# Performance work log

Hardware: AMD Instinct MI355X
Metric: run time of the kernel (lower is better)

## Reference

```python
import jax, jax.numpy as jnp
import numpy as np

EPS = 1e-6
DIAG_SIZE = 128  # triu band half-width (init kwarg diag_size)
NEG_INF = -1e9


def feature_map(x):
    # tanh feature map: phi(x) = tanh(x) + 1 (positive feature map)
    return jnp.tanh(x) + 1.0


def causal_dot_product(Q, K, V):
    # Q,K: [N,L,H,E], V: [N,L,H,D]
    # running KV state: S_l = sum_{s<=l} K_s V_s^T, materialized via cumsum
    kv = jnp.cumsum(jnp.einsum('nlhe,nlhd->nlhed', K, V), axis=1)  # [N,L,H,E,D]
    return jnp.einsum('nlhe,nlhed->nlhd', Q, kv)


def setup_inputs() -> dict:
    key = jax.random.key(0)
    k1, k2, k3 = jax.random.split(key, 3)
    N, L, H, E = 2, 2048, 8, 64
    queries = jax.random.normal(k1, (N, L, H, E), dtype=jnp.float32)
    keys = jax.random.normal(k2, (N, L, H, E), dtype=jnp.float32)
    values = jax.random.normal(k3, (N, L, H, E), dtype=jnp.float32)
    key_lengths_mask = jnp.ones((N, L), dtype=jnp.float32)  # all keys valid
    blend = jnp.full((1,), 0.9, dtype=jnp.float32)  # learned blend param (init 0.9)
    return {"queries": queries, "keys": keys, "values": values,
            "key_lengths_mask": key_lengths_mask, "blend": blend}


def reference(queries, keys, values, key_lengths_mask, blend):
    N, L, H, E = queries.shape
    # ---- linear attention path (kernel_1 = tanh, kernel_2 = 'none') ----
    Q1 = feature_map(queries)
    K1 = feature_map(keys) * key_lengths_mask[:, :, None, None]
    Z1 = 1.0 / (jnp.einsum('nlhi,nlhi->nlh', Q1, jnp.cumsum(K1, axis=1)) + EPS)
    LV = causal_dot_product(Q1, K1, values) * Z1[..., None]  # [N,L,H,D]
    # ---- full softmax attention path (banded by triu) ----
    softmax_temp = 1.0 / np.sqrt(E).astype(np.float32)
    QK = jnp.einsum('nlhe,nshe->nhls', queries, keys)  # [N,H,L,L]
    l_idx = jnp.arange(L)[:, None]
    s_idx = jnp.arange(L)[None, :]
    causal_add = jnp.where(s_idx <= l_idx, 0.0, NEG_INF)  # lower-triangular mask
    key_add = jnp.where(key_lengths_mask > 0, 0.0, NEG_INF)  # [N,L]
    logits = softmax_temp * (QK + causal_add[None, None] + key_add[:, None, None, :])
    A = jax.nn.softmax(logits, axis=-1)
    # torch.triu(A, diagonal=-diag_size): keep s >= l - diag_size
    band = s_idx >= (l_idx - DIAG_SIZE)
    A = jnp.where(band[None, None], A, 0.0)
    # dropout: eval mode (identity)
    SV = jnp.einsum('nhls,nshd->nlhd', A, values)
    b = blend[0]
    return b * SV + (1.0 - b) * LV
```

## Files before the change

### kernel.cpp

```cpp
#include <hip/hip_runtime.h>
#include <math.h>

#define N_ 2
#define L_ 2048
#define H_ 8
#define E_ 64
#define D_ 64
#define C_ 128
#define NC (L_/C_)
#define ROWSTRIDE (H_*E_)
#define TEMP 0.125f
#define EPS_F 1e-6f
#define NEG_INF_F (-1e9f)
#define CHUNK_WS (E_*D_ + E_)
#define NCHUNKS (N_*H_*NC)
#define TPAD 136
#define PPAD 72

typedef __attribute__((ext_vector_type(8))) short short8;
typedef __attribute__((ext_vector_type(4))) float f32x4;

__device__ __forceinline__ short f2bf(float x) {
  unsigned u = __float_as_uint(x);
  u += 0x7fffu + ((u >> 16) & 1u);
  return (short)(u >> 16);
}
__device__ __forceinline__ float bf2f(short s) {
  return __uint_as_float(((unsigned)(unsigned short)s) << 16);
}
__device__ __forceinline__ float tanh1f(float x) {
  float e = __expf(-2.f * x);
  return 2.f * __builtin_amdgcn_rcpf(1.f + e);
}

template <typename F>
__device__ __forceinline__ void stage_tile(short* __restrict__ dst,
                                           const float* __restrict__ src, F f) {
  const int t = threadIdx.x;
#pragma unroll
  for (int it = 0; it < 4; ++it) {
    int gi = it * 256 + t;
    int row = gi >> 3, g = gi & 7;
    const float* p = src + row * ROWSTRIDE + g * 8;
    float4 a = *(const float4*)p;
    float4 b = *(const float4*)(p + 4);
    float xs[8] = {a.x, a.y, a.z, a.w, b.x, b.y, b.z, b.w};
    short8 v;
#pragma unroll
    for (int j = 0; j < 8; ++j) v[j] = f2bf(f(xs[j], row));
    *(short8*)(dst + row * 64 + (g ^ (row & 7)) * 8) = v;
  }
}

__device__ __forceinline__ void stage_vT(short* __restrict__ vt,
                                         const float* __restrict__ Vbase) {
  const int t = threadIdx.x;
  const int d = t & 63, sb = t >> 6;
#pragma unroll
  for (int q = 0; q < 4; ++q) {
    int s0 = sb * 32 + q * 8;
    short8 v;
#pragma unroll
    for (int j = 0; j < 8; ++j) v[j] = f2bf(Vbase[(s0 + j) * ROWSTRIDE + d]);
    *(short8*)(vt + d * TPAD + (s0 >> 3) * 8) = v;
  }
}

__device__ __forceinline__ short8 frag_ld(const short* __restrict__ buf,
                                          int rowbase, int hf, int lane) {
  int r = rowbase + (lane & 15);
  int g = (hf * 4 + (lane >> 4)) ^ (r & 7);
  return *(const short8*)(buf + r * 64 + g * 8);
}
__device__ __forceinline__ short8 frag_ldT(const short* __restrict__ buf,
                                           int nbase, int g, int lane) {
  int r = nbase + (lane & 15);
  return *(const short8*)(buf + r * TPAD + g * 8);
}
__device__ __forceinline__ short8 frag_ldP(const short* __restrict__ buf,
                                           int rowbase, int ks, int lane) {
  int r = rowbase + (lane & 15);
  int g = ks * 4 + (lane >> 4);
  return *(const short8*)(buf + r * PPAD + g * 8);
}

__device__ __forceinline__ void pv_and_store(f32x4 acc[2][8], short* __restrict__ vt,
                                             short* __restrict__ pb,
                                             float* __restrict__ outp,
                                             int w, int lane, bool prevband) {
  const int col_lo = lane & 15;
  f32x4 accPV[2][4];
#pragma unroll
  for (int m = 0; m < 2; ++m)
#pragma unroll
    for (int nn = 0; nn < 4; ++nn) accPV[m][nn] = (f32x4){0.f, 0.f, 0.f, 0.f};
#pragma unroll
  for (int hh = 0; hh < 2; ++hh) {
#pragma unroll
    for (int m = 0; m < 2; ++m) {
      const int rbase = 32 * w + 16 * m + ((lane >> 4) << 2);
#pragma unroll
      for (int ch = 0; ch < 4; ++ch) {
        int ct = 4 * hh + ch, col = 16 * ct + col_lo;
#pragma unroll
        for (int reg = 0; reg < 4; ++reg) {
          float pp = acc[m][ct][reg];
          if (prevband && col < rbase + reg) pp = 0.f;
          pb[(rbase + reg) * PPAD + 16 * ch + col_lo] = f2bf(pp);
        }
      }
    }
#pragma unroll
    for (int ks = 0; ks < 2; ++ks) {
      short8 ap[2];
#pragma unroll
      for (int m = 0; m < 2; ++m) ap[m] = frag_ldP(pb, 32 * w + 16 * m, ks, lane);
      short8 bv[4];
#pragma unroll
      for (int nn = 0; nn < 4; ++nn)
        bv[nn] = frag_ldT(vt, 16 * nn, 8 * hh + ks * 4 + (lane >> 4), lane);
#pragma unroll
      for (int m = 0; m < 2; ++m)
#pragma unroll
        for (int nn = 0; nn < 4; ++nn)
          accPV[m][nn] = __builtin_amdgcn_mfma_f32_16x16x32_bf16(ap[m], bv[nn], accPV[m][nn], 0, 0, 0);
    }
  }
#pragma unroll
  for (int m = 0; m < 2; ++m) {
    const int rbase = 32 * w + 16 * m + ((lane >> 4) << 2);
#pragma unroll
    for (int nn = 0; nn < 4; ++nn)
#pragma unroll
      for (int reg = 0; reg < 4; ++reg)
        outp[(rbase + reg) * D_ + 16 * nn + col_lo] = accPV[m][nn][reg];
  }
}

extern "C" __global__ void __launch_bounds__(256, 3)
k_pre(const float* __restrict__ Q, const float* __restrict__ K,
      const float* __restrict__ V, const float* __restrict__ mask,
      float* __restrict__ ws, float* __restrict__ part,
      float* __restrict__ pvd, float* __restrict__ pvp,
      float* __restrict__ lvl, float* __restrict__ rsuml) {
  __shared__ short lds[17920];
  __shared__ float fmsk[C_];
  const int orig = blockIdx.x;
  const int swz = (orig & 7) * 336 + (orig >> 3);
  const int t = threadIdx.x;
  const int w = t >> 6, lane = t & 63;
  const int col_lo = lane & 15;

  if (swz < 2176) {
    const int nh = swz / 136;
    const int p = swz - nh * 136;
    int qb = (int)((sqrtf(8.f * p + 1.f) - 1.f) * 0.5f);
    while ((qb + 1) * (qb + 2) / 2 <= p) ++qb;
    while (qb * (qb + 1) / 2 > p) --qb;
    const int kb = p - qb * (qb + 1) / 2;
    const int h = nh & (H_ - 1), n = nh >> 3;
    const int koff = ((n * L_ + kb * C_) * H_ + h) * E_;

    stage_tile(lds, Q + ((n * L_ + qb * C_) * H_ + h) * E_,
               [](float x, int) { return x; });
    stage_tile(lds + 8192, K + koff, [](float x, int) { return x; });
    if (t < C_) fmsk[t] = mask[n * L_ + kb * C_ + t];
    __syncthreads();

    const int rowbase = w * 32;
    short8 afr[2][2];
#pragma unroll
    for (int m = 0; m < 2; ++m)
#pragma unroll
      for (int hh = 0; hh < 2; ++hh)
        afr[m][hh] = frag_ld(lds, rowbase + 16 * m, hh, lane);

    f32x4 acc[2][8];
#pragma unroll
    for (int m = 0; m < 2; ++m)
#pragma unroll
      for (int c = 0; c < 8; ++c) acc[m][c] = (f32x4){0.f, 0.f, 0.f, 0.f};
#pragma unroll
    for (int c = 0; c < 8; ++c) {
      short8 b0 = frag_ld(lds + 8192, 16 * c, 0, lane);
      short8 b1 = frag_ld(lds + 8192, 16 * c, 1, lane);
#pragma unroll
      for (int m = 0; m < 2; ++m) {
        acc[m][c] = __builtin_amdgcn_mfma_f32_16x16x32_bf16(afr[m][0], b0, acc[m][c], 0, 0, 0);
        acc[m][c] = __builtin_amdgcn_mfma_f32_16x16x32_bf16(afr[m][1], b1, acc[m][c], 0, 0, 0);
      }
    }

    const bool diag = (kb == qb), prev = (kb == qb - 1);
    float* pout = part + (size_t)(nh * NC + qb) * C_ * 16;
#pragma unroll
    for (int m = 0; m < 2; ++m) {
      const int rbase = rowbase + 16 * m + ((lane >> 4) << 2);
      float rs[4] = {0.f, 0.f, 0.f, 0.f};
#pragma unroll
      for (int c = 0; c < 8; ++c) {
        const int col = 16 * c + col_lo;
        const float madd = (fmsk[col] > 0.f) ? 0.f : NEG_INF_F;
#pragma unroll
        for (int reg = 0; reg < 4; ++reg) {
          float x = acc[m][c][reg] + madd;
          if (diag && col > rbase + reg) x += NEG_INF_F;
          float e = __expf(x * TEMP);
          acc[m][c][reg] = e;
          rs[reg] += e;
        }
      }
#pragma unroll
      for (int off = 1; off < 16; off <<= 1) {
#pragma unroll
        for (int reg = 0; reg < 4; ++reg) rs[reg] += __shfl_xor(rs[reg], off);
      }
      if (col_lo == 0) {
#pragma unroll
        for (int reg = 0; reg < 4; ++reg) pout[(rbase + reg) * 16 + kb] = rs[reg];
      }
    }

    if (diag || prev) {
      __syncthreads();
      stage_vT(lds, V + koff);
      __syncthreads();
      float* outp = (diag ? pvd : pvp) + (size_t)(nh * NC + qb) * (C_ * D_);
      pv_and_store(acc, lds, lds + 8704, outp, w, lane, prev);
    }
  } else if (swz < 2432) {
    const int id = swz - 2176;
    const int nh = id >> 4, c = id & 15;
    const int h = nh & (H_ - 1), n = nh >> 3;
    const int gbase = ((n * L_ + c * C_) * H_ + h) * E_;
    const int e = t & 63, sb = t >> 6;
    const int mbase = n * L_ + c * C_;
    short* k1T = lds;
    short* vT2 = lds + 8704;
#pragma unroll
    for (int q = 0; q < 4; ++q) {
      int s0 = sb * 32 + q * 8;
      short8 kk, vv;
#pragma unroll
      for (int j = 0; j < 8; ++j) {
        float kx = K[gbase + (s0 + j) * ROWSTRIDE + e];
        kk[j] = f2bf(tanh1f(kx) * mask[mbase + s0 + j]);
        vv[j] = f2bf(V[gbase + (s0 + j) * ROWSTRIDE + e]);
      }
      *(short8*)(k1T + e * TPAD + (s0 >> 3) * 8) = kk;
      *(short8*)(vT2 + e * TPAD + (s0 >> 3) * 8) = vv;
    }
    __syncthreads();

    f32x4 acc[4];
#pragma unroll
    for (int nn = 0; nn < 4; ++nn) acc[nn] = (f32x4){0.f, 0.f, 0.f, 0.f};
#pragma unroll
    for (int ks = 0; ks < 4; ++ks) {
      short8 a = frag_ldT(vT2, 16 * w, ks * 4 + (lane >> 4), lane);
#pragma unroll
      for (int nn = 0; nn < 4; ++nn) {
        short8 b = frag_ldT(k1T, 16 * nn, ks * 4 + (lane >> 4), lane);
        acc[nn] = __builtin_amdgcn_mfma_f32_16x16x32_bf16(a, b, acc[nn], 0, 0, 0);
      }
    }
    float* wsc = ws + (size_t)(nh * NC + c) * CHUNK_WS;
    const int drow = 16 * w + ((lane >> 4) << 2);
#pragma unroll
    for (int nn = 0; nn < 4; ++nn)
#pragma unroll
      for (int reg = 0; reg < 4; ++reg)
        wsc[(16 * nn + col_lo) * D_ + drow + reg] = acc[nn][reg];
    if (t < 64) {
      float s = 0.f;
#pragma unroll
      for (int g = 0; g < 16; ++g) {
        short8 v = *(const short8*)(k1T + t * TPAD + g * 8);
#pragma unroll
        for (int j = 0; j < 8; ++j) s += bf2f(v[j]);
      }
      wsc[E_ * D_ + t] = s;
    }
  } else {
    const int id = swz - 2432;
    const int nh = id >> 4, qb = id & 15;
    const int h = nh & (H_ - 1), n = nh >> 3;
    const int gbase = ((n * L_ + qb * C_) * H_ + h) * E_;
    const float* mrow = mask + n * L_ + qb * C_;

    stage_tile(lds, Q + gbase, [](float x, int) { return tanh1f(x); });
    stage_tile(lds + 8192, K + gbase,
               [mrow](float x, int row) { return tanh1f(x) * mrow[row]; });
    __syncthreads();

    const int rowbase = w * 32;
    short8 afr[2][2];
#pragma unroll
    for (int m = 0; m < 2; ++m)
#pragma unroll
      for (int hh = 0; hh < 2; ++hh)
        afr[m][hh] = frag_ld(lds, rowbase + 16 * m, hh, lane);

    f32x4 acc[2][8];
#pragma unroll
    for (int m = 0; m < 2; ++m)
#pragma unroll
      for (int c = 0; c < 8; ++c) acc[m][c] = (f32x4){0.f, 0.f, 0.f, 0.f};
#pragma unroll
    for (int c = 0; c < 8; ++c) {
      short8 b0 = frag_ld(lds + 8192, 16 * c, 0, lane);
      short8 b1 = frag_ld(lds + 8192, 16 * c, 1, lane);
#pragma unroll
      for (int m = 0; m < 2; ++m) {
        acc[m][c] = __builtin_amdgcn_mfma_f32_16x16x32_bf16(afr[m][0], b0, acc[m][c], 0, 0, 0);
        acc[m][c] = __builtin_amdgcn_mfma_f32_16x16x32_bf16(afr[m][1], b1, acc[m][c], 0, 0, 0);
      }
    }
    float* rout = rsuml + (size_t)(nh * NC + qb) * C_;
#pragma unroll
    for (int m = 0; m < 2; ++m) {
      const int rbase = rowbase + 16 * m + ((lane >> 4) << 2);
      float rs[4] = {0.f, 0.f, 0.f, 0.f};
#pragma unroll
      for (int c = 0; c < 8; ++c) {
        const int col = 16 * c + col_lo;
#pragma unroll
        for (int reg = 0; reg < 4; ++reg) {
          if (col <= rbase + reg) rs[reg] += acc[m][c][reg];
          else acc[m][c][reg] = 0.f;
        }
      }
#pragma unroll
      for (int off = 1; off < 16; off <<= 1) {
#pragma unroll
        for (int reg = 0; reg < 4; ++reg) rs[reg] += __shfl_xor(rs[reg], off);
      }
      if (col_lo == 0) {
#pragma unroll
        for (int reg = 0; reg < 4; ++reg) rout[rbase + reg] = rs[reg];
      }
    }
    __syncthreads();
    stage_vT(lds, V + gbase);
    __syncthreads();
    pv_and_store(acc, lds, lds + 8704,
                 lvl + (size_t)(nh * NC + qb) * (C_ * D_), w, lane, false);
  }
}

extern "C" __global__ void __launch_bounds__(256)
k_scan(float* __restrict__ ws) {
  const int bid = blockIdx.x;
  const int swz = (bid & 7) * 34 + (bid >> 3);
  const int nh = swz / 17, seg = swz - nh * 17;
  const int idx = seg * 256 + threadIdx.x;
  if (idx >= CHUNK_WS) return;
  float* base = ws + (size_t)nh * NC * CHUNK_WS + idx;
  float v[NC];
#pragma unroll
  for (int c = 0; c < NC; ++c) v[c] = base[(size_t)c * CHUNK_WS];
  float acc = 0.f;
#pragma unroll
  for (int c = 0; c < NC; ++c) {
    base[(size_t)c * CHUNK_WS] = acc;
    acc += v[c];
  }
}

extern "C" __global__ void __launch_bounds__(256)
k_fused(const float* __restrict__ Q, const float* __restrict__ blend,
        const float* __restrict__ ws, const float* __restrict__ part,
        const float* __restrict__ pvd, const float* __restrict__ pvp,
        const float* __restrict__ lvl, const float* __restrict__ rsuml,
        float* __restrict__ out) {
  __shared__ short kv[64 * TPAD];
  __shared__ float zlds[64];
  __shared__ float dinv[64];
  __shared__ float ksum[E_];

  const int orig = blockIdx.x;
  const int swz = (orig & 7) * 64 + (orig >> 3);
  const int rh = swz & 1, qb = (swz >> 1) & (NC - 1), nh = swz >> 5;
  const int h = nh & (H_ - 1), n = nh >> 3;
  const int t = threadIdx.x;
  const int w = t >> 6, lane = t & 63;
  const int rowbase = w * 16;
  const int col_lo = lane & 15;
  const int rb = rowbase + ((lane >> 4) << 2);
  const int rtile0 = rh * 64 + rb;
  const int qgbase = ((n * L_ + qb * C_ + rh * 64) * H_ + h) * E_;
  const float* wsc = ws + (size_t)(nh * NC + qb) * CHUNK_WS;
  const float bl = blend[0];
  const float ob = 1.f - bl;
  const int d = t & 63;
  const size_t tb = (size_t)(nh * NC + qb) * (C_ * D_);

  short8 af1[2];
  {
    const float* qp = Q + qgbase + (rowbase + (lane & 15)) * ROWSTRIDE;
#pragma unroll
    for (int kh = 0; kh < 2; ++kh) {
      int c0 = (kh * 4 + (lane >> 4)) * 8;
      float4 a = *(const float4*)(qp + c0);
      float4 b = *(const float4*)(qp + c0 + 4);
      float xs[8] = {a.x, a.y, a.z, a.w, b.x, b.y, b.z, b.w};
#pragma unroll
      for (int j = 0; j < 8; ++j) af1[kh][j] = f2bf(tanh1f(xs[j]));
    }
  }
  {
    int eb = t >> 6;
#pragma unroll
    for (int q = 0; q < 2; ++q) {
      int e0 = eb * 16 + q * 8;
      short8 v;
#pragma unroll
      for (int j = 0; j < 8; ++j) v[j] = f2bf(wsc[(e0 + j) * D_ + d]);
      *(short8*)(kv + d * TPAD + (e0 >> 3) * 8) = v;
    }
  }
  if (t < 64) {
    ksum[t] = wsc[E_ * D_ + t];
    const float* pb = part + ((size_t)(nh * NC + qb) * C_ + rh * 64 + t) * 16;
    float4 a = *(const float4*)pb, b = *(const float4*)(pb + 4);
    float4 c = *(const float4*)(pb + 8), d4 = *(const float4*)(pb + 12);
    float vv[16] = {a.x, a.y, a.z, a.w, b.x, b.y, b.z, b.w,
                    c.x, c.y, c.z, c.w, d4.x, d4.y, d4.z, d4.w};
    float s = 0.f;
#pragma unroll
    for (int j = 0; j < 16; ++j) s += (j <= qb) ? vv[j] : 0.f;
    dinv[t] = 1.f / s;
  }
  float rsv[4];
#pragma unroll
  for (int reg = 0; reg < 4; ++reg)
    rsv[reg] = rsuml[(size_t)(nh * NC + qb) * C_ + rtile0 + reg];
  float lvv[4][4], pvv[4][4];
#pragma unroll
  for (int nn = 0; nn < 4; ++nn)
#pragma unroll
    for (int reg = 0; reg < 4; ++reg) {
      size_t a = tb + (size_t)(rtile0 + reg) * D_ + 16 * nn + col_lo;
      lvv[nn][reg] = lvl[a];
      float pd = pvd[a];
      pvv[nn][reg] = (qb > 0) ? pd + pvp[a] : pd;
    }
  __syncthreads();

  {
    float zz = 0.f;
#pragma unroll
    for (int kh = 0; kh < 2; ++kh) {
      int cb = (kh * 4 + (lane >> 4)) * 8;
#pragma unroll
      for (int j = 0; j < 8; ++j) zz += bf2f(af1[kh][j]) * ksum[cb + j];
    }
    zz += __shfl_xor(zz, 16);
    zz += __shfl_xor(zz, 32);
    if (lane < 16) zlds[rowbase + lane] = zz;
  }
  f32x4 accL[4];
#pragma unroll
  for (int nn = 0; nn < 4; ++nn) accL[nn] = (f32x4){0.f, 0.f, 0.f, 0.f};
#pragma unroll
  for (int ks = 0; ks < 2; ++ks) {
    short8 bf[4];
#pragma unroll
    for (int nn = 0; nn < 4; ++nn)
      bf[nn] = frag_ldT(kv, 16 * nn, ks * 4 + (lane >> 4), lane);
#pragma unroll
    for (int nn = 0; nn < 4; ++nn)
      accL[nn] = __builtin_amdgcn_mfma_f32_16x16x32_bf16(af1[ks], bf[nn], accL[nn], 0, 0, 0);
  }

  float zrf[4], sdv[4];
#pragma unroll
  for (int reg = 0; reg < 4; ++reg) {
    zrf[reg] = ob / (zlds[rb + reg] + rsv[reg] + EPS_F);
    sdv[reg] = bl * dinv[rb + reg];
  }
#pragma unroll
  for (int nn = 0; nn < 4; ++nn)
#pragma unroll
    for (int reg = 0; reg < 4; ++reg)
      out[qgbase + (rb + reg) * ROWSTRIDE + 16 * nn + col_lo] =
          zrf[reg] * (accL[nn][reg] + lvv[nn][reg]) + sdv[reg] * pvv[nn][reg];
}

extern "C" void kernel_launch(void* const* d_in, const int* in_sizes, int n_in,
                              void* d_out, int out_size, void* d_ws, size_t ws_size,
                              hipStream_t stream) {
  (void)in_sizes; (void)n_in; (void)out_size; (void)ws_size;
  const float* Q = (const float*)d_in[0];
  const float* K = (const float*)d_in[1];
  const float* V = (const float*)d_in[2];
  const float* mask = (const float*)d_in[3];
  const float* blend = (const float*)d_in[4];
  float* out = (float*)d_out;
  float* ws = (float*)d_ws;
  float* part  = ws + (size_t)NCHUNKS * CHUNK_WS;
  float* pvd   = part + (size_t)NCHUNKS * C_ * 16;
  float* pvp   = pvd + (size_t)NCHUNKS * C_ * D_;
  float* lvl   = pvp + (size_t)NCHUNKS * C_ * D_;
  float* rsuml = lvl + (size_t)NCHUNKS * C_ * D_;

  k_pre<<<dim3(2688), dim3(256), 0, stream>>>(Q, K, V, mask, ws, part, pvd, pvp, lvl, rsuml);
  k_scan<<<dim3(272), dim3(256), 0, stream>>>(ws);
  k_fused<<<dim3(N_ * H_ * NC * 2), dim3(256), 0, stream>>>(Q, blend, ws, part, pvd, pvp, lvl, rsuml, out);
}
```

Baseline: 55.90 us.

## Interleave score MFMA, exp and PV per column half to cut registers

Restructures k_pre so the QK^T product is computed one 16-column tile at a time, immediately exponentiated and written to LDS as bf16, then multiplied by V for each 64-column half. This replaces the full 2x8 accumulator array and the separate pv_and_store pass. V is staged up front into a dedicated LDS buffer alongside Q and K, which removes the extra barriers and the serialized V staging. The block-to-work mapping is also regrouped per head (168 blocks each) rather than by task type, and the launch_bounds occupancy hint is dropped. Peak register pressure should fall, but LDS use per block rises, which may limit occupancy.

```diff
diff --git a/kernel.cpp b/kernel.cpp
--- a/kernel.cpp
+++ b/kernel.cpp
@@ -84,159 +84,128 @@
   return *(const short8*)(buf + r * PPAD + g * 8);
 }
 
-__device__ __forceinline__ void pv_and_store(f32x4 acc[2][8], short* __restrict__ vt,
-                                             short* __restrict__ pb,
-                                             float* __restrict__ outp,
-                                             int w, int lane, bool prevband) {
-  const int col_lo = lane & 15;
-  f32x4 accPV[2][4];
-#pragma unroll
-  for (int m = 0; m < 2; ++m)
-#pragma unroll
-    for (int nn = 0; nn < 4; ++nn) accPV[m][nn] = (f32x4){0.f, 0.f, 0.f, 0.f};
-#pragma unroll
-  for (int hh = 0; hh < 2; ++hh) {
-#pragma unroll
-    for (int m = 0; m < 2; ++m) {
-      const int rbase = 32 * w + 16 * m + ((lane >> 4) << 2);
-#pragma unroll
-      for (int ch = 0; ch < 4; ++ch) {
-        int ct = 4 * hh + ch, col = 16 * ct + col_lo;
-#pragma unroll
-        for (int reg = 0; reg < 4; ++reg) {
-          float pp = acc[m][ct][reg];
-          if (prevband && col < rbase + reg) pp = 0.f;
-          pb[(rbase + reg) * PPAD + 16 * ch + col_lo] = f2bf(pp);
-        }
-      }
-    }
-#pragma unroll
-    for (int ks = 0; ks < 2; ++ks) {
-      short8 ap[2];
-#pragma unroll
-      for (int m = 0; m < 2; ++m) ap[m] = frag_ldP(pb, 32 * w + 16 * m, ks, lane);
-      short8 bv[4];
-#pragma unroll
-      for (int nn = 0; nn < 4; ++nn)
-        bv[nn] = frag_ldT(vt, 16 * nn, 8 * hh + ks * 4 + (lane >> 4), lane);
-#pragma unroll
-      for (int m = 0; m < 2; ++m)
-#pragma unroll
-        for (int nn = 0; nn < 4; ++nn)
-          accPV[m][nn] = __builtin_amdgcn_mfma_f32_16x16x32_bf16(ap[m], bv[nn], accPV[m][nn], 0, 0, 0);
-    }
-  }
-#pragma unroll
-  for (int m = 0; m < 2; ++m) {
-    const int rbase = 32 * w + 16 * m + ((lane >> 4) << 2);
-#pragma unroll
-    for (int nn = 0; nn < 4; ++nn)
-#pragma unroll
-      for (int reg = 0; reg < 4; ++reg)
-        outp[(rbase + reg) * D_ + 16 * nn + col_lo] = accPV[m][nn][reg];
-  }
-}
-
-extern "C" __global__ void __launch_bounds__(256, 3)
+extern "C" __global__ void __launch_bounds__(256)
 k_pre(const float* __restrict__ Q, const float* __restrict__ K,
       const float* __restrict__ V, const float* __restrict__ mask,
       float* __restrict__ ws, float* __restrict__ part,
       float* __restrict__ pvd, float* __restrict__ pvp,
       float* __restrict__ lvl, float* __restrict__ rsuml) {
-  __shared__ short lds[17920];
+  __shared__ short ldsA[9216];
+  __shared__ short ldsB[8192];
+  __shared__ short ldsC[8704];
   __shared__ float fmsk[C_];
   const int orig = blockIdx.x;
   const int swz = (orig & 7) * 336 + (orig >> 3);
+  const int nh = swz / 168;
+  const int r = swz - nh * 168;
+  const int h = nh & (H_ - 1), n = nh >> 3;
   const int t = threadIdx.x;
   const int w = t >> 6, lane = t & 63;
   const int col_lo = lane & 15;
 
-  if (swz < 2176) {
-    const int nh = swz / 136;
-    const int p = swz - nh * 136;
+  if (r < 136) {
+    const int p = r;
     int qb = (int)((sqrtf(8.f * p + 1.f) - 1.f) * 0.5f);
     while ((qb + 1) * (qb + 2) / 2 <= p) ++qb;
     while (qb * (qb + 1) / 2 > p) --qb;
     const int kb = p - qb * (qb + 1) / 2;
-    const int h = nh & (H_ - 1), n = nh >> 3;
+    const bool diag = (kb == qb), prev = (kb == qb - 1), band = diag || prev;
     const int koff = ((n * L_ + kb * C_) * H_ + h) * E_;
 
-    stage_tile(lds, Q + ((n * L_ + qb * C_) * H_ + h) * E_,
+    stage_tile(ldsA, Q + ((n * L_ + qb * C_) * H_ + h) * E_,
                [](float x, int) { return x; });
-    stage_tile(lds + 8192, K + koff, [](float x, int) { return x; });
+    stage_tile(ldsB, K + koff, [](float x, int) { return x; });
+    if (band) stage_vT(ldsC, V + koff);
     if (t < C_) fmsk[t] = mask[n * L_ + kb * C_ + t];
     __syncthreads();
 
-    const int rowbase = w * 32;
     short8 afr[2][2];
 #pragma unroll
     for (int m = 0; m < 2; ++m)
 #pragma unroll
-      for (int hh = 0; hh < 2; ++hh)
-        afr[m][hh] = frag_ld(lds, rowbase + 16 * m, hh, lane);
-
-    f32x4 acc[2][8];
+      for (int hf = 0; hf < 2; ++hf)
+        afr[m][hf] = frag_ld(ldsA, w * 32 + 16 * m, hf, lane);
+    __syncthreads();
+
+    float rs[2][4] = {};
+    f32x4 accPV[2][4];
 #pragma unroll
     for (int m = 0; m < 2; ++m)
 #pragma unroll
-      for (int c = 0; c < 8; ++c) acc[m][c] = (f32x4){0.f, 0.f, 0.f, 0.f};
-#pragma unroll
-    for (int c = 0; c < 8; ++c) {
-      short8 b0 = frag_ld(lds + 8192, 16 * c, 0, lane);
-      short8 b1 = frag_ld(lds + 8192, 16 * c, 1, lane);
+      for (int nn = 0; nn < 4; ++nn) accPV[m][nn] = (f32x4){0.f, 0.f, 0.f, 0.f};
+
+#pragma unroll
+    for (int hh = 0; hh < 2; ++hh) {
+#pragma unroll
+      for (int cc = 0; cc < 4; ++cc) {
+        const int ct = hh * 4 + cc;
+        short8 b0 = frag_ld(ldsB, 16 * ct, 0, lane);
+        short8 b1 = frag_ld(ldsB, 16 * ct, 1, lane);
+        const int col = 16 * ct + col_lo;
+        const float madd = (fmsk[col] > 0.f) ? 0.f : NEG_INF_F;
+#pragma unroll
+        for (int m = 0; m < 2; ++m) {
+          f32x4 c = (f32x4){0.f, 0.f, 0.f, 0.f};
+          c = __builtin_amdgcn_mfma_f32_16x16x32_bf16(afr[m][0], b0, c, 0, 0, 0);
+          c = __builtin_amdgcn_mfma_f32_16x16x32_bf16(afr[m][1], b1, c, 0, 0, 0);
+          const int rbase = w * 32 + 16 * m + ((lane >> 4) << 2);
+#pragma unroll
+          for (int reg = 0; reg < 4; ++reg) {
+            float x = c[reg] + madd;
+            if (diag && col > rbase + reg) x += NEG_INF_F;
+            float e = __expf(x * TEMP);
+            rs[m][reg] += e;
+            if (band) {
+              if (prev && col < rbase + reg) e = 0.f;
+              ldsA[(rbase + reg) * PPAD + cc * 16 + col_lo] = f2bf(e);
+            }
+          }
+        }
+      }
+      if (band) {
+#pragma unroll
+        for (int ks = 0; ks < 2; ++ks) {
+          short8 ap0 = frag_ldP(ldsA, w * 32, ks, lane);
+          short8 ap1 = frag_ldP(ldsA, w * 32 + 16, ks, lane);
+#pragma unroll
+          for (int nn = 0; nn < 4; ++nn) {
+            short8 bv = frag_ldT(ldsC, 16 * nn, 8 * hh + ks * 4 + (lane >> 4), lane);
+            accPV[0][nn] = __builtin_amdgcn_mfma_f32_16x16x32_bf16(ap0, bv, accPV[0][nn], 0, 0, 0);
+            accPV[1][nn] = __builtin_amdgcn_mfma_f32_16x16x32_bf16(ap1, bv, accPV[1][nn], 0, 0, 0);
+          }
+        }
+      }
+    }
+    float* pout = part + (size_t)(nh * NC + qb) * C_ * 16;
+#pragma unroll
+    for (int m = 0; m < 2; ++m) {
+#pragma unroll
+      for (int off = 1; off < 16; off <<= 1)
+#pragma unroll
+        for (int reg = 0; reg < 4; ++reg) rs[m][reg] += __shfl_xor(rs[m][reg], off);
+      if (col_lo == 0) {
+        const int rbase = w * 32 + 16 * m + ((lane >> 4) << 2);
+#pragma unroll
+        for (int reg = 0; reg < 4; ++reg) pout[(rbase + reg) * 16 + kb] = rs[m][reg];
+      }
+    }
+    if (band) {
+      float* outp = (diag ? pvd : pvp) + (size_t)(nh * NC + qb) * (C_ * D_);
 #pragma unroll
       for (int m = 0; m < 2; ++m) {
-        acc[m][c] = __builtin_amdgcn_mfma_f32_16x16x32_bf16(afr[m][0], b0, acc[m][c], 0, 0, 0);
-        acc[m][c] = __builtin_amdgcn_mfma_f32_16x16x32_bf16(afr[m][1], b1, acc[m][c], 0, 0, 0);
-      }
-    }
-
-    const bool diag = (kb == qb), prev = (kb == qb - 1);
-    float* pout = part + (size_t)(nh * NC + qb) * C_ * 16;
-#pragma unroll
-    for (int m = 0; m < 2; ++m) {
-      const int rbase = rowbase + 16 * m + ((lane >> 4) << 2);
-      float rs[4] = {0.f, 0.f, 0.f, 0.f};
-#pragma unroll
-      for (int c = 0; c < 8; ++c) {
-        const int col = 16 * c + col_lo;
-        const float madd = (fmsk[col] > 0.f) ? 0.f : NEG_INF_F;
-#pragma unroll
-        for (int reg = 0; reg < 4; ++reg) {
-          float x = acc[m][c][reg] + madd;
-          if (diag && col > rbase + reg) x += NEG_INF_F;
-          float e = __expf(x * TEMP);
-          acc[m][c][reg] = e;
-          rs[reg] += e;
-        }
-      }
-#pragma unroll
-      for (int off = 1; off < 16; off <<= 1) {
-#pragma unroll
-        for (int reg = 0; reg < 4; ++reg) rs[reg] += __shfl_xor(rs[reg], off);
-      }
-      if (col_lo == 0) {
-#pragma unroll
-        for (int reg = 0; reg < 4; ++reg) pout[(rbase + reg) * 16 + kb] = rs[reg];
-      }
-    }
-
-    if (diag || prev) {
-      __syncthreads();
-      stage_vT(lds, V + koff);
-      __syncthreads();
-      float* outp = (diag ? pvd : pvp) + (size_t)(nh * NC + qb) * (C_ * D_);
-      pv_and_store(acc, lds, lds + 8704, outp, w, lane, prev);
-    }
-  } else if (swz < 2432) {
-    const int id = swz - 2176;
-    const int nh = id >> 4, c = id & 15;
-    const int h = nh & (H_ - 1), n = nh >> 3;
+        const int rbase = w * 32 + 16 * m + ((lane >> 4) << 2);
+#pragma unroll
+        for (int nn = 0; nn < 4; ++nn)
+#pragma unroll
+          for (int reg = 0; reg < 4; ++reg)
+            outp[(rbase + reg) * D_ + 16 * nn + col_lo] = accPV[m][nn][reg];
+      }
+    }
+  } else if (r < 152) {
+    const int c = r - 136;
     const int gbase = ((n * L_ + c * C_) * H_ + h) * E_;
     const int e = t & 63, sb = t >> 6;
     const int mbase = n * L_ + c * C_;
-    short* k1T = lds;
-    short* vT2 = lds + 8704;
 #pragma unroll
     for (int q = 0; q < 4; ++q) {
       int s0 = sb * 32 + q * 8;
@@ -247,8 +216,8 @@
         kk[j] = f2bf(tanh1f(kx) * mask[mbase + s0 + j]);
         vv[j] = f2bf(V[gbase + (s0 + j) * ROWSTRIDE + e]);
       }
-      *(short8*)(k1T + e * TPAD + (s0 >> 3) * 8) = kk;
-      *(short8*)(vT2 + e * TPAD + (s0 >> 3) * 8) = vv;
+      *(short8*)(ldsA + e * TPAD + (s0 >> 3) * 8) = kk;
+      *(short8*)(ldsC + e * TPAD + (s0 >> 3) * 8) = vv;
     }
     __syncthreads();
 
@@ -257,10 +226,10 @@
     for (int nn = 0; nn < 4; ++nn) acc[nn] = (f32x4){0.f, 0.f, 0.f, 0.f};
 #pragma unroll
     for (int ks = 0; ks < 4; ++ks) {
-      short8 a = frag_ldT(vT2, 16 * w, ks * 4 + (lane >> 4), lane);
+      short8 a = frag_ldT(ldsC, 16 * w, ks * 4 + (lane >> 4), lane);
 #pragma unroll
       for (int nn = 0; nn < 4; ++nn) {
-        short8 b = frag_ldT(k1T, 16 * nn, ks * 4 + (lane >> 4), lane);
+        short8 b = frag_ldT(ldsA, 16 * nn, ks * 4 + (lane >> 4), lane);
         acc[nn] = __builtin_amdgcn_mfma_f32_16x16x32_bf16(a, b, acc[nn], 0, 0, 0);
       }
     }
@@ -275,76 +244,96 @@
       float s = 0.f;
 #pragma unroll
       for (int g = 0; g < 16; ++g) {
-        short8 v = *(const short8*)(k1T + t * TPAD + g * 8);
+        short8 v = *(const short8*)(ldsA + t * TPAD + g * 8);
 #pragma unroll
         for (int j = 0; j < 8; ++j) s += bf2f(v[j]);
       }
       wsc[E_ * D_ + t] = s;
     }
   } else {
-    const int id = swz - 2432;
-    const int nh = id >> 4, qb = id & 15;
-    const int h = nh & (H_ - 1), n = nh >> 3;
+    const int qb = r - 152;
     const int gbase = ((n * L_ + qb * C_) * H_ + h) * E_;
     const float* mrow = mask + n * L_ + qb * C_;
 
-    stage_tile(lds, Q + gbase, [](float x, int) { return tanh1f(x); });
-    stage_tile(lds + 8192, K + gbase,
+    stage_tile(ldsA, Q + gbase, [](float x, int) { return tanh1f(x); });
+    stage_tile(ldsB, K + gbase,
                [mrow](float x, int row) { return tanh1f(x) * mrow[row]; });
+    stage_vT(ldsC, V + gbase);
     __syncthreads();
 
-    const int rowbase = w * 32;
     short8 afr[2][2];
 #pragma unroll
     for (int m = 0; m < 2; ++m)
 #pragma unroll
-      for (int hh = 0; hh < 2; ++hh)
-        afr[m][hh] = frag_ld(lds, rowbase + 16 * m, hh, lane);
-
-    f32x4 acc[2][8];
+      for (int hf = 0; hf < 2; ++hf)
+        afr[m][hf] = frag_ld(ldsA, w * 32 + 16 * m, hf, lane);
+    __syncthreads();
+
+    float rs[2][4] = {};
+    f32x4 accPV[2][4];
 #pragma unroll
     for (int m = 0; m < 2; ++m)
 #pragma unroll
-      for (int c = 0; c < 8; ++c) acc[m][c] = (f32x4){0.f, 0.f, 0.f, 0.f};
-#pragma unroll
-    for (int c = 0; c < 8; ++c) {
-      short8 b0 = frag_ld(lds + 8192, 16 * c, 0, lane);
-      short8 b1 = frag_ld(lds + 8192, 16 * c, 1, lane);
-#pragma unroll
-      for (int m = 0; m < 2; ++m) {
-        acc[m][c] = __builtin_amdgcn_mfma_f32_16x16x32_bf16(afr[m][0], b0, acc[m][c], 0, 0, 0);
-        acc[m][c] = __builtin_amdgcn_mfma_f32_16x16x32_bf16(afr[m][1], b1, acc[m][c], 0, 0, 0);
+      for (int nn = 0; nn < 4; ++nn) accPV[m][nn] = (f32x4){0.f, 0.f, 0.f, 0.f};
+
+#pragma unroll
+    for (int hh = 0; hh < 2; ++hh) {
+#pragma unroll
+      for (int cc = 0; cc < 4; ++cc) {
+        const int ct = hh * 4 + cc;
+        short8 b0 = frag_ld(ldsB, 16 * ct, 0, lane);
+        short8 b1 = frag_ld(ldsB, 16 * ct, 1, lane);
+        const int col = 16 * ct + col_lo;
+#pragma unroll
+        for (int m = 0; m < 2; ++m) {
+          f32x4 c = (f32x4){0.f, 0.f, 0.f, 0.f};
+          c = __builtin_amdgcn_mfma_f32_16x16x32_bf16(afr[m][0], b0, c, 0, 0, 0);
+          c = __builtin_amdgcn_mfma_f32_16x16x32_bf16(afr[m][1], b1, c, 0, 0, 0);
+          const int rbase = w * 32 + 16 * m + ((lane >> 4) << 2);
+#pragma unroll
+          for (int reg = 0; reg < 4; ++reg) {
+            float v = c[reg];
+            if (col <= rbase + reg) rs[m][reg] += v;
+            else v = 0.f;
+            ldsA[(rbase + reg) * PPAD + cc * 16 + col_lo] = f2bf(v);
+          }
+        }
+      }
+#pragma unroll
+      for (int ks = 0; ks < 2; ++ks) {
+        short8 ap0 = frag_ldP(ldsA, w * 32, ks, lane);
+        short8 ap1 = frag_ldP(ldsA, w * 32 + 16, ks, lane);
+#pragma unroll
+        for (int nn = 0; nn < 4; ++nn) {
+          short8 bv = frag_ldT(ldsC, 16 * nn, 8 * hh + ks * 4 + (lane >> 4), lane);
+          accPV[0][nn] = __builtin_amdgcn_mfma_f32_16x16x32_bf16(ap0, bv, accPV[0][nn], 0, 0, 0);
+          accPV[1][nn] = __builtin_amdgcn_mfma_f32_16x16x32_bf16(ap1, bv, accPV[1][nn], 0, 0, 0);
+        }
       }
     }
     float* rout = rsuml + (size_t)(nh * NC + qb) * C_;
 #pragma unroll
     for (int m = 0; m < 2; ++m) {
-      const int rbase = rowbase + 16 * m + ((lane >> 4) << 2);
-      float rs[4] = {0.f, 0.f, 0.f, 0.f};
-#pragma unroll
-      for (int c = 0; c < 8; ++c) {
-        const int col = 16 * c + col_lo;
-#pragma unroll
-        for (int reg = 0; reg < 4; ++reg) {
-          if (col <= rbase + reg) rs[reg] += acc[m][c][reg];
-          else acc[m][c][reg] = 0.f;
-        }
-      }
-#pragma unroll
-      for (int off = 1; off < 16; off <<= 1) {
-#pragma unroll
-        for (int reg = 0; reg < 4; ++reg) rs[reg] += __shfl_xor(rs[reg], off);
-      }
+#pragma unroll
+      for (int off = 1; off < 16; off <<= 1)
+#pragma unroll
+        for (int reg = 0; reg < 4; ++reg) rs[m][reg] += __shfl_xor(rs[m][reg], off);
       if (col_lo == 0) {
-#pragma unroll
-        for (int reg = 0; reg < 4; ++reg) rout[rbase + reg] = rs[reg];
-      }
-    }
-    __syncthreads();
-    stage_vT(lds, V + gbase);
-    __syncthreads();
-    pv_and_store(acc, lds, lds + 8704,
-                 lvl + (size_t)(nh * NC + qb) * (C_ * D_), w, lane, false);
+        const int rbase = w * 32 + 16 * m + ((lane >> 4) << 2);
+#pragma unroll
+        for (int reg = 0; reg < 4; ++reg) rout[rbase + reg] = rs[m][reg];
+      }
+    }
+    float* outp = lvl + (size_t)(nh * NC + qb) * (C_ * D_);
+#pragma unroll
+    for (int m = 0; m < 2; ++m) {
+      const int rbase = w * 32 + 16 * m + ((lane >> 4) << 2);
+#pragma unroll
+      for (int nn = 0; nn < 4; ++nn)
+#pragma unroll
+        for (int reg = 0; reg < 4; ++reg)
+          outp[(rbase + reg) * D_ + 16 * nn + col_lo] = accPV[m][nn][reg];
+    }
   }
 }
 
@@ -368,11 +357,11 @@
 }
 
 extern "C" __global__ void __launch_bounds__(256)
-k_fused(const float* __restrict__ Q, const float* __restrict__ blend,
-        const float* __restrict__ ws, const float* __restrict__ part,
-        const float* __restrict__ pvd, const float* __restrict__ pvp,
-        const float* __restrict__ lvl, const float* __restrict__ rsuml,
-        float* __restrict__ out) {
+k_comb(const float* __restrict__ Q, const float* __restrict__ blend,
+       const float* __restrict__ ws, const float* __restrict__ part,
+       const float* __restrict__ pvd, const float* __restrict__ pvp,
+       const float* __restrict__ lvl, const float* __restrict__ rsuml,
+       float* __restrict__ out) {
   __shared__ short kv[64 * TPAD];
   __shared__ float zlds[64];
   __shared__ float dinv[64];
@@ -506,5 +495,5 @@
 
   k_pre<<<dim3(2688), dim3(256), 0, stream>>>(Q, K, V, mask, ws, part, pvd, pvp, lvl, rsuml);
   k_scan<<<dim3(272), dim3(256), 0, stream>>>(ws);
-  k_fused<<<dim3(N_ * H_ * NC * 2), dim3(256), 0, stream>>>(Q, blend, ws, part, pvd, pvp, lvl, rsuml, out);
-}
+  k_comb<<<dim3(512), dim3(256), 0, stream>>>(Q, blend, ws, part, pvd, pvp, lvl, rsuml, out);
+}
```

Result: no change. 55.06 us (-1.5%).

## Split band and intra-chunk linear PV work into separate half-tile kernel

Applied to the files above, without the earlier changes.

Moves the banded softmax PV (diagonal and previous chunk) and the intra-chunk linear-attention PV out of k_pre into a new k_bandlin kernel. That kernel processes 64-row half tiles, loading Q fragments straight from global memory. k_pre now only computes softmax row-sum partials and chunk KV states, with lighter blocks and no occupancy hint. The aim is to even out load imbalance, since a few heavy blocks in the triangular grid did extra PV work. The cost is an extra kernel launch, and K and V tiles are re-staged in both kernels.

```diff
diff --git a/kernel.cpp b/kernel.cpp
--- a/kernel.cpp
+++ b/kernel.cpp
@@ -84,69 +84,15 @@
   return *(const short8*)(buf + r * PPAD + g * 8);
 }
 
-__device__ __forceinline__ void pv_and_store(f32x4 acc[2][8], short* __restrict__ vt,
-                                             short* __restrict__ pb,
-                                             float* __restrict__ outp,
-                                             int w, int lane, bool prevband) {
-  const int col_lo = lane & 15;
-  f32x4 accPV[2][4];
-#pragma unroll
-  for (int m = 0; m < 2; ++m)
-#pragma unroll
-    for (int nn = 0; nn < 4; ++nn) accPV[m][nn] = (f32x4){0.f, 0.f, 0.f, 0.f};
-#pragma unroll
-  for (int hh = 0; hh < 2; ++hh) {
-#pragma unroll
-    for (int m = 0; m < 2; ++m) {
-      const int rbase = 32 * w + 16 * m + ((lane >> 4) << 2);
-#pragma unroll
-      for (int ch = 0; ch < 4; ++ch) {
-        int ct = 4 * hh + ch, col = 16 * ct + col_lo;
-#pragma unroll
-        for (int reg = 0; reg < 4; ++reg) {
-          float pp = acc[m][ct][reg];
-          if (prevband && col < rbase + reg) pp = 0.f;
-          pb[(rbase + reg) * PPAD + 16 * ch + col_lo] = f2bf(pp);
-        }
-      }
-    }
-#pragma unroll
-    for (int ks = 0; ks < 2; ++ks) {
-      short8 ap[2];
-#pragma unroll
-      for (int m = 0; m < 2; ++m) ap[m] = frag_ldP(pb, 32 * w + 16 * m, ks, lane);
-      short8 bv[4];
-#pragma unroll
-      for (int nn = 0; nn < 4; ++nn)
-        bv[nn] = frag_ldT(vt, 16 * nn, 8 * hh + ks * 4 + (lane >> 4), lane);
-#pragma unroll
-      for (int m = 0; m < 2; ++m)
-#pragma unroll
-        for (int nn = 0; nn < 4; ++nn)
-          accPV[m][nn] = __builtin_amdgcn_mfma_f32_16x16x32_bf16(ap[m], bv[nn], accPV[m][nn], 0, 0, 0);
-    }
-  }
-#pragma unroll
-  for (int m = 0; m < 2; ++m) {
-    const int rbase = 32 * w + 16 * m + ((lane >> 4) << 2);
-#pragma unroll
-    for (int nn = 0; nn < 4; ++nn)
-#pragma unroll
-      for (int reg = 0; reg < 4; ++reg)
-        outp[(rbase + reg) * D_ + 16 * nn + col_lo] = accPV[m][nn][reg];
-  }
-}
-
-extern "C" __global__ void __launch_bounds__(256, 3)
+extern "C" __global__ void __launch_bounds__(256)
 k_pre(const float* __restrict__ Q, const float* __restrict__ K,
       const float* __restrict__ V, const float* __restrict__ mask,
-      float* __restrict__ ws, float* __restrict__ part,
-      float* __restrict__ pvd, float* __restrict__ pvp,
-      float* __restrict__ lvl, float* __restrict__ rsuml) {
-  __shared__ short lds[17920];
+      float* __restrict__ ws, float* __restrict__ part) {
+  __shared__ short ldsA[64 * TPAD];
+  __shared__ short ldsB[64 * TPAD];
   __shared__ float fmsk[C_];
   const int orig = blockIdx.x;
-  const int swz = (orig & 7) * 336 + (orig >> 3);
+  const int swz = (orig & 7) * 304 + (orig >> 3);
   const int t = threadIdx.x;
   const int w = t >> 6, lane = t & 63;
   const int col_lo = lane & 15;
@@ -159,11 +105,11 @@
     while (qb * (qb + 1) / 2 > p) --qb;
     const int kb = p - qb * (qb + 1) / 2;
     const int h = nh & (H_ - 1), n = nh >> 3;
-    const int koff = ((n * L_ + kb * C_) * H_ + h) * E_;
-
-    stage_tile(lds, Q + ((n * L_ + qb * C_) * H_ + h) * E_,
+
+    stage_tile(ldsA, Q + ((n * L_ + qb * C_) * H_ + h) * E_,
                [](float x, int) { return x; });
-    stage_tile(lds + 8192, K + koff, [](float x, int) { return x; });
+    stage_tile(ldsB, K + ((n * L_ + kb * C_) * H_ + h) * E_,
+               [](float x, int) { return x; });
     if (t < C_) fmsk[t] = mask[n * L_ + kb * C_ + t];
     __syncthreads();
 
@@ -173,17 +119,18 @@
     for (int m = 0; m < 2; ++m)
 #pragma unroll
       for (int hh = 0; hh < 2; ++hh)
-        afr[m][hh] = frag_ld(lds, rowbase + 16 * m, hh, lane);
+        afr[m][hh] = frag_ld(ldsA, rowbase + 16 * m, hh, lane);
 
     f32x4 acc[2][8];
 #pragma unroll
     for (int m = 0; m < 2; ++m)
 #pragma unroll
       for (int c = 0; c < 8; ++c) acc[m][c] = (f32x4){0.f, 0.f, 0.f, 0.f};
+
 #pragma unroll
     for (int c = 0; c < 8; ++c) {
-      short8 b0 = frag_ld(lds + 8192, 16 * c, 0, lane);
-      short8 b1 = frag_ld(lds + 8192, 16 * c, 1, lane);
+      short8 b0 = frag_ld(ldsB, 16 * c, 0, lane);
+      short8 b1 = frag_ld(ldsB, 16 * c, 1, lane);
 #pragma unroll
       for (int m = 0; m < 2; ++m) {
         acc[m][c] = __builtin_amdgcn_mfma_f32_16x16x32_bf16(afr[m][0], b0, acc[m][c], 0, 0, 0);
@@ -191,7 +138,7 @@
       }
     }
 
-    const bool diag = (kb == qb), prev = (kb == qb - 1);
+    const bool diag = (kb == qb);
     float* pout = part + (size_t)(nh * NC + qb) * C_ * 16;
 #pragma unroll
     for (int m = 0; m < 2; ++m) {
@@ -205,9 +152,7 @@
         for (int reg = 0; reg < 4; ++reg) {
           float x = acc[m][c][reg] + madd;
           if (diag && col > rbase + reg) x += NEG_INF_F;
-          float e = __expf(x * TEMP);
-          acc[m][c][reg] = e;
-          rs[reg] += e;
+          rs[reg] += __expf(x * TEMP);
         }
       }
 #pragma unroll
@@ -220,23 +165,13 @@
         for (int reg = 0; reg < 4; ++reg) pout[(rbase + reg) * 16 + kb] = rs[reg];
       }
     }
-
-    if (diag || prev) {
-      __syncthreads();
-      stage_vT(lds, V + koff);
-      __syncthreads();
-      float* outp = (diag ? pvd : pvp) + (size_t)(nh * NC + qb) * (C_ * D_);
-      pv_and_store(acc, lds, lds + 8704, outp, w, lane, prev);
-    }
-  } else if (swz < 2432) {
+  } else {
     const int id = swz - 2176;
     const int nh = id >> 4, c = id & 15;
     const int h = nh & (H_ - 1), n = nh >> 3;
     const int gbase = ((n * L_ + c * C_) * H_ + h) * E_;
     const int e = t & 63, sb = t >> 6;
     const int mbase = n * L_ + c * C_;
-    short* k1T = lds;
-    short* vT2 = lds + 8704;
 #pragma unroll
     for (int q = 0; q < 4; ++q) {
       int s0 = sb * 32 + q * 8;
@@ -247,8 +182,8 @@
         kk[j] = f2bf(tanh1f(kx) * mask[mbase + s0 + j]);
         vv[j] = f2bf(V[gbase + (s0 + j) * ROWSTRIDE + e]);
       }
-      *(short8*)(k1T + e * TPAD + (s0 >> 3) * 8) = kk;
-      *(short8*)(vT2 + e * TPAD + (s0 >> 3) * 8) = vv;
+      *(short8*)(ldsA + e * TPAD + (s0 >> 3) * 8) = kk;
+      *(short8*)(ldsB + e * TPAD + (s0 >> 3) * 8) = vv;
     }
     __syncthreads();
 
@@ -257,10 +192,10 @@
     for (int nn = 0; nn < 4; ++nn) acc[nn] = (f32x4){0.f, 0.f, 0.f, 0.f};
 #pragma unroll
     for (int ks = 0; ks < 4; ++ks) {
-      short8 a = frag_ldT(vT2, 16 * w, ks * 4 + (lane >> 4), lane);
+      short8 a = frag_ldT(ldsB, 16 * w, ks * 4 + (lane >> 4), lane);
 #pragma unroll
       for (int nn = 0; nn < 4; ++nn) {
-        short8 b = frag_ldT(k1T, 16 * nn, ks * 4 + (lane >> 4), lane);
+        short8 b = frag_ldT(ldsA, 16 * nn, ks * 4 + (lane >> 4), lane);
         acc[nn] = __builtin_amdgcn_mfma_f32_16x16x32_bf16(a, b, acc[nn], 0, 0, 0);
       }
     }
@@ -275,77 +210,153 @@
       float s = 0.f;
 #pragma unroll
       for (int g = 0; g < 16; ++g) {
-        short8 v = *(const short8*)(k1T + t * TPAD + g * 8);
+        short8 v = *(const short8*)(ldsA + t * TPAD + g * 8);
 #pragma unroll
         for (int j = 0; j < 8; ++j) s += bf2f(v[j]);
       }
       wsc[E_ * D_ + t] = s;
     }
+  }
+}
+
+extern "C" __global__ void __launch_bounds__(256)
+k_bandlin(const float* __restrict__ Q, const float* __restrict__ K,
+          const float* __restrict__ V, const float* __restrict__ mask,
+          float* __restrict__ pvd, float* __restrict__ pvp,
+          float* __restrict__ lvl, float* __restrict__ rsuml) {
+  __shared__ short kbuf[C_ * 64];
+  __shared__ short vt[64 * TPAD];
+  __shared__ short pbuf[64 * PPAD];
+  __shared__ float fmsk[C_];
+  const int orig = blockIdx.x;
+  const int swz = (orig & 7) * 192 + (orig >> 3);
+  const int nh = swz / 96, r = swz - nh * 96;
+  const int h = nh & (H_ - 1), n = nh >> 3;
+  const int t = threadIdx.x;
+  const int w = t >> 6, lane = t & 63;
+  const int col_lo = lane & 15;
+  const int prow = w * 16 + ((lane >> 4) << 2);
+
+  const bool isband = (r < 64);
+  int qb, rh, kb;
+  bool diag = false;
+  if (isband) {
+    qb = r >> 2; rh = (r >> 1) & 1;
+    const int slot = r & 1;
+    diag = (slot == 0);
+    kb = diag ? qb : qb - 1;
+    if (!diag && qb == 0) return;
   } else {
-    const int id = swz - 2432;
-    const int nh = id >> 4, qb = id & 15;
-    const int h = nh & (H_ - 1), n = nh >> 3;
-    const int gbase = ((n * L_ + qb * C_) * H_ + h) * E_;
-    const float* mrow = mask + n * L_ + qb * C_;
-
-    stage_tile(lds, Q + gbase, [](float x, int) { return tanh1f(x); });
-    stage_tile(lds + 8192, K + gbase,
+    const int r2 = r - 64;
+    qb = r2 >> 1; rh = r2 & 1; kb = qb;
+  }
+
+  const int koff = ((n * L_ + kb * C_) * H_ + h) * E_;
+  const int qoff = ((n * L_ + qb * C_ + rh * 64) * H_ + h) * E_;
+  const float* mrow = mask + n * L_ + kb * C_;
+
+  if (isband) {
+    stage_tile(kbuf, K + koff, [](float x, int) { return x; });
+    if (t < C_) fmsk[t] = mrow[t];
+  } else {
+    stage_tile(kbuf, K + koff,
                [mrow](float x, int row) { return tanh1f(x) * mrow[row]; });
-    __syncthreads();
-
-    const int rowbase = w * 32;
-    short8 afr[2][2];
-#pragma unroll
-    for (int m = 0; m < 2; ++m)
-#pragma unroll
-      for (int hh = 0; hh < 2; ++hh)
-        afr[m][hh] = frag_ld(lds, rowbase + 16 * m, hh, lane);
-
-    f32x4 acc[2][8];
-#pragma unroll
-    for (int m = 0; m < 2; ++m)
-#pragma unroll
-      for (int c = 0; c < 8; ++c) acc[m][c] = (f32x4){0.f, 0.f, 0.f, 0.f};
-#pragma unroll
-    for (int c = 0; c < 8; ++c) {
-      short8 b0 = frag_ld(lds + 8192, 16 * c, 0, lane);
-      short8 b1 = frag_ld(lds + 8192, 16 * c, 1, lane);
-#pragma unroll
-      for (int m = 0; m < 2; ++m) {
-        acc[m][c] = __builtin_amdgcn_mfma_f32_16x16x32_bf16(afr[m][0], b0, acc[m][c], 0, 0, 0);
-        acc[m][c] = __builtin_amdgcn_mfma_f32_16x16x32_bf16(afr[m][1], b1, acc[m][c], 0, 0, 0);
-      }
-    }
-    float* rout = rsuml + (size_t)(nh * NC + qb) * C_;
-#pragma unroll
-    for (int m = 0; m < 2; ++m) {
-      const int rbase = rowbase + 16 * m + ((lane >> 4) << 2);
-      float rs[4] = {0.f, 0.f, 0.f, 0.f};
-#pragma unroll
-      for (int c = 0; c < 8; ++c) {
-        const int col = 16 * c + col_lo;
-#pragma unroll
-        for (int reg = 0; reg < 4; ++reg) {
-          if (col <= rbase + reg) rs[reg] += acc[m][c][reg];
-          else acc[m][c][reg] = 0.f;
-        }
-      }
-#pragma unroll
-      for (int off = 1; off < 16; off <<= 1) {
-#pragma unroll
-        for (int reg = 0; reg < 4; ++reg) rs[reg] += __shfl_xor(rs[reg], off);
-      }
-      if (col_lo == 0) {
-#pragma unroll
-        for (int reg = 0; reg < 4; ++reg) rout[rbase + reg] = rs[reg];
-      }
-    }
-    __syncthreads();
-    stage_vT(lds, V + gbase);
-    __syncthreads();
-    pv_and_store(acc, lds, lds + 8704,
-                 lvl + (size_t)(nh * NC + qb) * (C_ * D_), w, lane, false);
-  }
+  }
+  stage_vT(vt, V + koff);
+  __syncthreads();
+
+  short8 af[2];
+  {
+    const float* qp = Q + qoff + (w * 16 + (lane & 15)) * ROWSTRIDE;
+#pragma unroll
+    for (int kh = 0; kh < 2; ++kh) {
+      int c0 = (kh * 4 + (lane >> 4)) * 8;
+      float4 a = *(const float4*)(qp + c0);
+      float4 b = *(const float4*)(qp + c0 + 4);
+      float xs[8] = {a.x, a.y, a.z, a.w, b.x, b.y, b.z, b.w};
+#pragma unroll
+      for (int j = 0; j < 8; ++j)
+        af[kh][j] = isband ? f2bf(xs[j]) : f2bf(tanh1f(xs[j]));
+    }
+  }
+
+  f32x4 acc[8];
+#pragma unroll
+  for (int ct = 0; ct < 8; ++ct) acc[ct] = (f32x4){0.f, 0.f, 0.f, 0.f};
+#pragma unroll
+  for (int ct = 0; ct < 8; ++ct) {
+    short8 b0 = frag_ld(kbuf, 16 * ct, 0, lane);
+    short8 b1 = frag_ld(kbuf, 16 * ct, 1, lane);
+    acc[ct] = __builtin_amdgcn_mfma_f32_16x16x32_bf16(af[0], b0, acc[ct], 0, 0, 0);
+    acc[ct] = __builtin_amdgcn_mfma_f32_16x16x32_bf16(af[1], b1, acc[ct], 0, 0, 0);
+  }
+
+  const int rowc = rh * 64 + prow;
+  float rs[4] = {0.f, 0.f, 0.f, 0.f};
+#pragma unroll
+  for (int ct = 0; ct < 8; ++ct) {
+    const int col = 16 * ct + col_lo;
+    if (isband) {
+      const float madd = (fmsk[col] > 0.f) ? 0.f : NEG_INF_F;
+#pragma unroll
+      for (int reg = 0; reg < 4; ++reg) {
+        float x = acc[ct][reg] + madd;
+        if (diag && col > rowc + reg) x += NEG_INF_F;
+        float e = __expf(x * TEMP);
+        if (!diag && col < rowc + reg) e = 0.f;
+        acc[ct][reg] = e;
+      }
+    } else {
+#pragma unroll
+      for (int reg = 0; reg < 4; ++reg) {
+        float v = acc[ct][reg];
+        if (col <= rowc + reg) rs[reg] += v;
+        else v = 0.f;
+        acc[ct][reg] = v;
+      }
+    }
+  }
+  if (!isband) {
+#pragma unroll
+    for (int off = 1; off < 16; off <<= 1)
+#pragma unroll
+      for (int reg = 0; reg < 4; ++reg) rs[reg] += __shfl_xor(rs[reg], off);
+    if (col_lo == 0) {
+      float* rout = rsuml + (size_t)(nh * NC + qb) * C_;
+#pragma unroll
+      for (int reg = 0; reg < 4; ++reg) rout[rowc + reg] = rs[reg];
+    }
+  }
+
+  f32x4 acc2[4];
+#pragma unroll
+  for (int nn = 0; nn < 4; ++nn) acc2[nn] = (f32x4){0.f, 0.f, 0.f, 0.f};
+#pragma unroll
+  for (int hh = 0; hh < 2; ++hh) {
+#pragma unroll
+    for (int cc = 0; cc < 4; ++cc) {
+      const int ct = 4 * hh + cc, colh = 16 * cc + col_lo;
+#pragma unroll
+      for (int reg = 0; reg < 4; ++reg)
+        pbuf[(prow + reg) * PPAD + colh] = f2bf(acc[ct][reg]);
+    }
+#pragma unroll
+    for (int ks = 0; ks < 2; ++ks) {
+      short8 ap = frag_ldP(pbuf, w * 16, ks, lane);
+#pragma unroll
+      for (int nn = 0; nn < 4; ++nn) {
+        short8 bv = frag_ldT(vt, 16 * nn, 8 * hh + ks * 4 + (lane >> 4), lane);
+        acc2[nn] = __builtin_amdgcn_mfma_f32_16x16x32_bf16(ap, bv, acc2[nn], 0, 0, 0);
+      }
+    }
+  }
+
+  float* outp = (isband ? (diag ? pvd : pvp) : lvl) + (size_t)(nh * NC + qb) * (C_ * D_);
+#pragma unroll
+  for (int nn = 0; nn < 4; ++nn)
+#pragma unroll
+    for (int reg = 0; reg < 4; ++reg)
+      outp[(size_t)(rowc + reg) * D_ + 16 * nn + col_lo] = acc2[nn][reg];
 }
 
 extern "C" __global__ void __launch_bounds__(256)
@@ -368,11 +379,11 @@
 }
 
 extern "C" __global__ void __launch_bounds__(256)
-k_fused(const float* __restrict__ Q, const float* __restrict__ blend,
-        const float* __restrict__ ws, const float* __restrict__ part,
-        const float* __restrict__ pvd, const float* __restrict__ pvp,
-        const float* __restrict__ lvl, const float* __restrict__ rsuml,
-        float* __restrict__ out) {
+k_comb(const float* __restrict__ Q, const float* __restrict__ blend,
+       const float* __restrict__ ws, const float* __restrict__ part,
+       const float* __restrict__ pvd, const float* __restrict__ pvp,
+       const float* __restrict__ lvl, const float* __restrict__ rsuml,
+       float* __restrict__ out) {
   __shared__ short kv[64 * TPAD];
   __shared__ float zlds[64];
   __shared__ float dinv[64];
@@ -504,7 +515,8 @@
   float* lvl   = pvp + (size_t)NCHUNKS * C_ * D_;
   float* rsuml = lvl + (size_t)NCHUNKS * C_ * D_;
 
-  k_pre<<<dim3(2688), dim3(256), 0, stream>>>(Q, K, V, mask, ws, part, pvd, pvp, lvl, rsuml);
+  k_bandlin<<<dim3(1536), dim3(256), 0, stream>>>(Q, K, V, mask, pvd, pvp, lvl, rsuml);
+  k_pre<<<dim3(2432), dim3(256), 0, stream>>>(Q, K, V, mask, ws, part);
   k_scan<<<dim3(272), dim3(256), 0, stream>>>(ws);
-  k_fused<<<dim3(N_ * H_ * NC * 2), dim3(256), 0, stream>>>(Q, blend, ws, part, pvd, pvp, lvl, rsuml, out);
-}
+  k_comb<<<dim3(512), dim3(256), 0, stream>>>(Q, blend, ws, part, pvd, pvp, lvl, rsuml, out);
+}
```

Result: slower. 58.67 us (+5.0%).
